# Kernel tuning notes

Hardware: AMD Instinct MI355X
Metric: run time of the kernel (lower is better)

The kernel has to match this reference:

```python
import jax, jax.numpy as jnp
import numpy as np

B, L0, L1, NS, D, H, NL, HM = 16, 512, 256, 32, 256, 8, 4, 4
T = L0 + L1 + NS + 1
HD = D // H
EPS = 1e-5
SCALE = HD ** -0.5


def setup_inputs() -> dict:
    key = jax.random.key(0)
    ks = jax.random.split(key, 20)
    s = 0.02
    return {
        'seq_tokens_0': jax.random.normal(ks[0], (B, L0, D), jnp.float32),
        'seq_tokens_1': jax.random.normal(ks[1], (B, L1, D), jnp.float32),
        'seq_lens_0': jax.random.randint(ks[2], (B,), 0, L0),
        'seq_lens_1': jax.random.randint(ks[3], (B,), 0, L1),
        'ns_tokens': jax.random.normal(ks[4], (B, NS, D), jnp.float32),
        'domain_emb': jax.random.normal(ks[5], (2, D), jnp.float32) * s,
        'cls_token': jax.random.normal(ks[6], (1, 1, D), jnp.float32) * s,
        'ln1_w': jnp.ones((NL, D), jnp.float32),
        'ln1_b': jnp.zeros((NL, D), jnp.float32),
        'qkv_w': jax.random.normal(ks[7], (NL, D, 3 * D), jnp.float32) * s,
        'qkv_b': jnp.zeros((NL, 3 * D), jnp.float32),
        'out_w': jax.random.normal(ks[8], (NL, D, D), jnp.float32) * s,
        'out_b': jnp.zeros((NL, D), jnp.float32),
        'ln2_w': jnp.ones((NL, D), jnp.float32),
        'ln2_b': jnp.zeros((NL, D), jnp.float32),
        'ffn1_w': jax.random.normal(ks[9], (NL, D, HM * D), jnp.float32) * s,
        'ffn1_b': jnp.zeros((NL, HM * D), jnp.float32),
        'ffn2_w': jax.random.normal(ks[10], (NL, HM * D, D), jnp.float32) * s,
        'ffn2_b': jnp.zeros((NL, D), jnp.float32),
        'fln_w': jnp.ones((D,), jnp.float32),
        'fln_b': jnp.zeros((D,), jnp.float32),
    }


def _ln(x, w, b):
    m = jnp.mean(x, -1, keepdims=True)
    v = jnp.var(x, -1, keepdims=True)
    return (x - m) * jax.lax.rsqrt(v + EPS) * w + b


def _build_mask(seq_lens_0, seq_lens_1):
    # static block structure: intra-domain causal, S<->NS bidirectional, CLS sink row
    base = jnp.zeros((T, T), bool)
    base = base.at[:L0, :L0].set(jnp.tril(jnp.ones((L0, L0), bool)))
    base = base.at[L0:L0 + L1, L0:L0 + L1].set(jnp.tril(jnp.ones((L1, L1), bool)))
    ns_s, ns_e = L0 + L1, L0 + L1 + NS
    base = base.at[:ns_s, ns_s:ns_e].set(True)   # S -> NS
    base = base.at[ns_s:ns_e, :ns_e].set(True)   # NS -> S and NS -> NS
    base = base.at[T - 1, :ns_e].set(True)       # CLS reads all S/NS
    base = base.at[T - 1, T - 1].set(True)       # CLS reads itself
    # per-batch padding mask on keys of each seq segment
    kv = jnp.ones((B, T), bool)
    kv = kv.at[:, :L0].set(jnp.arange(L0)[None, :] < seq_lens_0[:, None])
    kv = kv.at[:, L0:L0 + L1].set(jnp.arange(L1)[None, :] < seq_lens_1[:, None])
    return base[None] & kv[:, None, :]  # [B, T, T]


def _attention(x, mask, qkv_w, qkv_b, out_w, out_b):
    qkv = (x @ qkv_w + qkv_b).reshape(B, T, 3, H, HD)
    q, k, v = qkv[:, :, 0], qkv[:, :, 1], qkv[:, :, 2]
    scores = jnp.einsum('bqhd,bkhd->bhqk', q, k) * SCALE
    m = mask[:, None]  # [B,1,T,T]
    s = jnp.where(m, scores, -jnp.inf)
    any_valid = jnp.any(m, -1, keepdims=True)
    mx = jnp.where(any_valid, jnp.max(s, -1, keepdims=True), 0.0)
    e = jnp.exp(s - mx)  # masked entries exp(-inf)=0
    denom = jnp.sum(e, -1, keepdims=True)
    probs = e / jnp.maximum(denom, 1e-30)  # fully-masked rows -> zeros
    out = jnp.einsum('bhqk,bkhd->bqhd', probs, v).reshape(B, T, D)
    return out @ out_w + out_b


def reference(seq_tokens_0, seq_tokens_1, seq_lens_0, seq_lens_1, ns_tokens,
              domain_emb, cls_token, ln1_w, ln1_b, qkv_w, qkv_b, out_w, out_b,
              ln2_w, ln2_b, ffn1_w, ffn1_b, ffn2_w, ffn2_b, fln_w, fln_b):
    t0 = seq_tokens_0 + domain_emb[0][None, None, :]
    t1 = seq_tokens_1 + domain_emb[1][None, None, :]
    cls = jnp.broadcast_to(cls_token, (B, 1, D))
    x = jnp.concatenate([t0, t1, ns_tokens, cls], axis=1)  # [B,T,D]
    mask = _build_mask(seq_lens_0, seq_lens_1)
    for l in range(NL):
        x = x + _attention(_ln(x, ln1_w[l], ln1_b[l]), mask,
                           qkv_w[l], qkv_b[l], out_w[l], out_b[l])
        h = _ln(x, ln2_w[l], ln2_b[l])
        h = jax.nn.gelu(h @ ffn1_w[l] + ffn1_b[l], approximate=False)
        x = x + h @ ffn2_w[l] + ffn2_b[l]
    x = _ln(x, fln_w, fln_b)
    return x[:, -1, :]  # CLS state [B,D]
```

## Files before the change

### kernel.cpp

```cpp
#include <hip/hip_runtime.h>
#include <hip/hip_bf16.h>
#include <math.h>

typedef __attribute__((ext_vector_type(8))) unsigned short ushort8;
typedef __attribute__((ext_vector_type(8))) short short8;
typedef __attribute__((ext_vector_type(4))) float f32x4;
typedef __attribute__((ext_vector_type(4))) unsigned short ushort4v;
typedef __attribute__((ext_vector_type(4))) int i32x4;
typedef unsigned int u32;

namespace {
constexpr int B = 16, L0 = 512, L1 = 256, NS = 32, D = 256, H = 8, NL = 4, HM = 4;
constexpr int T = L0 + L1 + NS + 1;
constexpr int HD = D / H;
constexpr int NTOK = B * T;
constexpr int NS_S = L0 + L1;
constexpr int NS_E = NS_S + NS;
constexpr int TPAD = 832;
constexpr float EPS = 1e-5f;
constexpr float SCL2  = 0.17677669529663687f * 1.4426950408889634f;
}

__device__ __forceinline__ ushort f2bf(float f) {
    union { float f; unsigned u; } v; v.f = f;
    return (ushort)((v.u + 0x7fffu + ((v.u >> 16) & 1u)) >> 16);
}

__device__ __forceinline__ u32 cvtpk(float a, float b) {
    u32 r;
    asm("v_cvt_pk_bf16_f32 %0, %1, %2" : "=v"(r) : "v"(a), "v"(b));
    return r;
}

__device__ __forceinline__ void gload_lds16(const void* g, void* l) {
    __builtin_amdgcn_global_load_lds(
        (const __attribute__((address_space(1))) u32*)g,
        (__attribute__((address_space(3))) u32*)l, 16, 0, 0);
}

__device__ __forceinline__ bool any_valid_rows(
    int m0, int rows, const int* __restrict__ len0, const int* __restrict__ len1)
{
    int m1 = m0 + rows; if (m1 > NTOK) m1 = NTOK;
    const int b0 = m0 / T, b1 = (m1 - 1) / T;
    for (int b = b0; b <= b1; ++b) {
        int t0 = m0 - b * T; if (t0 < 0) t0 = 0;
        int t1 = m1 - b * T; if (t1 > T) t1 = T;
        if (t0 < len0[b]) return true;
        if (t1 > L0 && t0 < L0 + len1[b]) return true;
        if (t1 > NS_S) return true;
    }
    return false;
}

__global__ __launch_bounds__(256) void k_wprep_all(
    const float* __restrict__ qkvw, const float* __restrict__ outw,
    const float* __restrict__ f1w, const float* __restrict__ f2w,
    ushort* __restrict__ qkvt, ushort* __restrict__ outt,
    ushort* __restrict__ f1t, ushort* __restrict__ f2t)
{
    int id = blockIdx.x;
    const float* src; ushort* dst; int K, N;
    if (id < 768)        { src = qkvw; dst = qkvt; K = 256;  N = 768;  }
    else if (id < 1024)  { id -= 768;  src = outw; dst = outt; K = 256; N = 256; }
    else if (id < 2048)  { id -= 1024; src = f1w;  dst = f1t;  K = 256; N = 1024; }
    else                 { id -= 2048; src = f2w;  dst = f2t;  K = 1024; N = 256; }
    const int ktiles = K >> 5, per = ktiles * (N >> 5);
    const int layer = id / per, rem = id % per;
    const int kb = (rem % ktiles) * 32, nb = (rem / ktiles) * 32;
    src += (size_t)layer * K * N; dst += (size_t)layer * K * N;

    __shared__ float t[32][33];
    const int c = threadIdx.x & 31, r8 = threadIdx.x >> 5;
#pragma unroll
    for (int rr = 0; rr < 32; rr += 8)
        t[r8 + rr][c] = src[(size_t)(kb + r8 + rr) * N + nb + c];
    __syncthreads();
#pragma unroll
    for (int rr = 0; rr < 32; rr += 8)
        dst[(size_t)(nb + r8 + rr) * K + kb + c] = f2bf(t[c][r8 + rr]);
}

__global__ __launch_bounds__(256) void k_build_ln(
    const float* __restrict__ s0, const float* __restrict__ s1,
    const float* __restrict__ ns, const float* __restrict__ dom,
    const float* __restrict__ cls, const float* __restrict__ lnw,
    const float* __restrict__ lnb, float* __restrict__ x, ushort* __restrict__ xn)
{
    const int wid = threadIdx.x >> 6, lane = threadIdx.x & 63;
    const int row = blockIdx.x * 4 + wid;
    if (row >= NTOK) return;
    const int b = row / T, t = row % T;
    const int d0 = lane * 4;
    float4 v;
    if (t < L0) {
        v = *(const float4*)(s0 + ((size_t)b * L0 + t) * D + d0);
        float4 dm = *(const float4*)(dom + d0);
        v.x += dm.x; v.y += dm.y; v.z += dm.z; v.w += dm.w;
    } else if (t < NS_S) {
        v = *(const float4*)(s1 + ((size_t)b * L1 + (t - L0)) * D + d0);
        float4 dm = *(const float4*)(dom + D + d0);
        v.x += dm.x; v.y += dm.y; v.z += dm.z; v.w += dm.w;
    } else if (t < NS_E) {
        v = *(const float4*)(ns + ((size_t)b * NS + (t - NS_S)) * D + d0);
    } else {
        v = *(const float4*)(cls + d0);
    }
    *(float4*)(x + (size_t)row * D + d0) = v;
    float s  = v.x + v.y + v.z + v.w;
    float ss = v.x * v.x + v.y * v.y + v.z * v.z + v.w * v.w;
#pragma unroll
    for (int o = 32; o; o >>= 1) { s += __shfl_xor(s, o); ss += __shfl_xor(ss, o); }
    const float mean = s * (1.f / D);
    const float var  = ss * (1.f / D) - mean * mean;
    const float r = rsqrtf(var + EPS);
    float4 wv = *(const float4*)(lnw + d0);
    float4 bv = *(const float4*)(lnb + d0);
    ushort4v o4;
    o4[0] = f2bf((v.x - mean) * r * wv.x + bv.x);
    o4[1] = f2bf((v.y - mean) * r * wv.y + bv.y);
    o4[2] = f2bf((v.z - mean) * r * wv.z + bv.z);
    o4[3] = f2bf((v.w - mean) * r * wv.w + bv.w);
    *(ushort4v*)(xn + (size_t)row * D + d0) = o4;
}

template<bool GELU, bool RES, bool OBF, bool CLSW>
__global__ __launch_bounds__(256) void k_gemm_mfma(
    const ushort* __restrict__ A, const ushort* __restrict__ Wt,
    const float* __restrict__ bias, void* __restrict__ Cout,
    const float* __restrict__ res, const int* __restrict__ len0,
    const int* __restrict__ len1, int M, int N, int K, int nOff)
{
    __shared__ ushort As[2][128 * 64];
    __shared__ ushort Bs[2][128 * 64];
    const int tid = threadIdx.x;
    const int lane = tid & 63, w = tid >> 6;
    const int lo = lane & 15, g = lane >> 4;
    const int wr = w >> 1, wc = w & 1;
    const int m0 = CLSW ? (((blockIdx.x * T + (T - 1)) >> 7) << 7) : blockIdx.x * 128;
    const int n0 = (blockIdx.y + nOff) * 128;

    if (!CLSW && !any_valid_rows(m0, 128, len0, len1)) return;

    f32x4 zero = {0.f, 0.f, 0.f, 0.f};
    f32x4 acc[4][4];
#pragma unroll
    for (int mi = 0; mi < 4; ++mi)
#pragma unroll
        for (int ni = 0; ni < 4; ++ni) acc[mi][ni] = zero;

    const ushort* srcA[4];
    const ushort* srcB[4];
    int ldsOff[4];
#pragma unroll
    for (int i = 0; i < 4; ++i) {
        const int idx16 = (w * 4 + i) * 64 + lane;
        const int row = idx16 >> 3;
        const int scb = ((idx16 & 7) * 16) ^ ((row & 7) << 4);
        int arow = m0 + row; if (arow >= M) arow = M - 1;
        srcA[i] = A  + (size_t)arow * K + (scb >> 1);
        srcB[i] = Wt + (size_t)(n0 + row) * K + (scb >> 1);
        ldsOff[i] = (w * 4 + i) * 512;
    }

    const int NT = K >> 6;
#pragma unroll
    for (int i = 0; i < 4; ++i) {
        gload_lds16(srcA[i], &As[0][ldsOff[i]]);
        gload_lds16(srcB[i], &Bs[0][ldsOff[i]]);
    }
    asm volatile("s_waitcnt vmcnt(0)");
    __syncthreads();

    for (int t = 0; t < NT; ++t) {
        const int buf = t & 1;
        if (t + 1 < NT) {
            const int nb = buf ^ 1, ko = (t + 1) * 64;
#pragma unroll
            for (int i = 0; i < 4; ++i) {
                gload_lds16(srcA[i] + ko, &As[nb][ldsOff[i]]);
                gload_lds16(srcB[i] + ko, &Bs[nb][ldsOff[i]]);
            }
        }
#pragma unroll
        for (int kk = 0; kk < 2; ++kk) {
            const int kb = (kk * 64 + g * 16) ^ ((lo & 7) << 4);
            short8 af[4], bfr[4];
#pragma unroll
            for (int mi = 0; mi < 4; ++mi)
                af[mi] = *(const short8*)&As[buf][(wr * 64 + mi * 16 + lo) * 64 + (kb >> 1)];
#pragma unroll
            for (int ni = 0; ni < 4; ++ni)
                bfr[ni] = *(const short8*)&Bs[buf][(wc * 64 + ni * 16 + lo) * 64 + (kb >> 1)];
#pragma unroll
            for (int mi = 0; mi < 4; ++mi)
#pragma unroll
                for (int ni = 0; ni < 4; ++ni)
                    acc[mi][ni] = __builtin_amdgcn_mfma_f32_16x16x32_bf16(
                        af[mi], bfr[ni], acc[mi][ni], 0, 0, 0);
        }
        asm volatile("s_waitcnt vmcnt(0)");
        __syncthreads();
    }

    float bv[4];
#pragma unroll
    for (int ni = 0; ni < 4; ++ni) bv[ni] = bias[n0 + wc * 64 + ni * 16 + lo];
#pragma unroll
    for (int mi = 0; mi < 4; ++mi) {
#pragma unroll
        for (int i = 0; i < 4; ++i) {
            const int row = m0 + wr * 64 + mi * 16 + g * 4 + i;
            if (row >= M) continue;
#pragma unroll
            for (int ni = 0; ni < 4; ++ni) {
                const int col = n0 + wc * 64 + ni * 16 + lo;
                float v = acc[mi][ni][i] + bv[ni];
                if (GELU) v = 0.5f * v * (1.0f + erff(v * 0.70710678118654752f));
                if (RES)  v += res[(size_t)row * N + col];
                if (OBF) ((ushort*)Cout)[(size_t)row * N + col] = f2bf(v);
                else     ((float*)Cout)[(size_t)row * N + col] = v;
            }
        }
    }
}

template<int MODE, bool CLSW>
__global__ __launch_bounds__(256) void k_gemm_fused(
    const ushort* __restrict__ A, const ushort* __restrict__ Wt,
    const float* __restrict__ bias, const float* __restrict__ res,
    const float* __restrict__ lnw, const float* __restrict__ lnb,
    float* __restrict__ xout, ushort* __restrict__ xnout,
    float* __restrict__ dout, const int* __restrict__ len0,
    const int* __restrict__ len1, int M, int K)
{
    __shared__ ushort As[2][64 * 64];
    __shared__ ushort Bs[2][256 * 64];
    __shared__ float redS[64][4];
    __shared__ float redQ[64][4];
    const int tid = threadIdx.x;
    const int lane = tid & 63, w = tid >> 6;
    const int lo = lane & 15, g = lane >> 4;
    const int m0 = CLSW ? (((blockIdx.x * T + (T - 1)) >> 6) << 6) : blockIdx.x * 64;

    if (!CLSW && !any_valid_rows(m0, 64, len0, len1)) return;

    f32x4 zero = {0.f, 0.f, 0.f, 0.f};
    f32x4 acc[4][4];
#pragma unroll
    for (int mi = 0; mi < 4; ++mi)
#pragma unroll
        for (int ni = 0; ni < 4; ++ni) acc[mi][ni] = zero;

    const ushort* srcA[2]; int ldsOffA[2];
    const ushort* srcB[8]; int ldsOffB[8];
#pragma unroll
    for (int j = 0; j < 2; ++j) {
        const int idx16 = j * 256 + tid;
        const int row = idx16 >> 3;
        const int scb = ((idx16 & 7) * 16) ^ ((row & 7) << 4);
        int arow = m0 + row; if (arow >= M) arow = M - 1;
        srcA[j] = A + (size_t)arow * K + (scb >> 1);
        ldsOffA[j] = idx16 * 8;
    }
#pragma unroll
    for (int j = 0; j < 8; ++j) {
        const int idx16 = j * 256 + tid;
        const int row = idx16 >> 3;
        const int scb = ((idx16 & 7) * 16) ^ ((row & 7) << 4);
        srcB[j] = Wt + (size_t)row * K + (scb >> 1);
        ldsOffB[j] = idx16 * 8;
    }

    const int NT = K >> 6;
#pragma unroll
    for (int j = 0; j < 2; ++j) gload_lds16(srcA[j], &As[0][ldsOffA[j]]);
#pragma unroll
    for (int j = 0; j < 8; ++j) gload_lds16(srcB[j], &Bs[0][ldsOffB[j]]);
    asm volatile("s_waitcnt vmcnt(0)");
    __syncthreads();

    for (int t = 0; t < NT; ++t) {
        const int buf = t & 1;
        if (t + 1 < NT) {
            const int nb = buf ^ 1, ko = (t + 1) * 64;
#pragma unroll
            for (int j = 0; j < 2; ++j) gload_lds16(srcA[j] + ko, &As[nb][ldsOffA[j]]);
#pragma unroll
            for (int j = 0; j < 8; ++j) gload_lds16(srcB[j] + ko, &Bs[nb][ldsOffB[j]]);
        }
#pragma unroll
        for (int kk = 0; kk < 2; ++kk) {
            const int kb = (kk * 64 + g * 16) ^ ((lo & 7) << 4);
            short8 af[4], bfr[4];
#pragma unroll
            for (int mi = 0; mi < 4; ++mi)
                af[mi] = *(const short8*)&As[buf][(mi * 16 + lo) * 64 + (kb >> 1)];
#pragma unroll
            for (int ni = 0; ni < 4; ++ni)
                bfr[ni] = *(const short8*)&Bs[buf][(w * 64 + ni * 16 + lo) * 64 + (kb >> 1)];
#pragma unroll
            for (int mi = 0; mi < 4; ++mi)
#pragma unroll
                for (int ni = 0; ni < 4; ++ni)
                    acc[mi][ni] = __builtin_amdgcn_mfma_f32_16x16x32_bf16(
                        af[mi], bfr[ni], acc[mi][ni], 0, 0, 0);
        }
        asm volatile("s_waitcnt vmcnt(0)");
        __syncthreads();
    }

    float bv[4], lw[4], lb[4];
#pragma unroll
    for (int ni = 0; ni < 4; ++ni) {
        const int c = w * 64 + ni * 16 + lo;
        bv[ni] = bias[c]; lw[ni] = lnw[c]; lb[ni] = lnb[c];
    }
#pragma unroll
    for (int mi = 0; mi < 4; ++mi) {
#pragma unroll
        for (int i = 0; i < 4; ++i) {
            const int r64 = mi * 16 + g * 4 + i;
            const int row = m0 + r64;
            float s = 0.f, q = 0.f;
            if (row < M) {
#pragma unroll
                for (int ni = 0; ni < 4; ++ni) {
                    const int col = w * 64 + ni * 16 + lo;
                    float v = acc[mi][ni][i] + bv[ni] + res[(size_t)row * 256 + col];
                    acc[mi][ni][i] = v;
                    s += v; q += v * v;
                }
                s += __shfl_xor(s, 1); q += __shfl_xor(q, 1);
                s += __shfl_xor(s, 2); q += __shfl_xor(q, 2);
                s += __shfl_xor(s, 4); q += __shfl_xor(q, 4);
                s += __shfl_xor(s, 8); q += __shfl_xor(q, 8);
                if (lo == 0) { redS[r64][w] = s; redQ[r64][w] = q; }
            }
        }
    }
    __syncthreads();
#pragma unroll
    for (int mi = 0; mi < 4; ++mi) {
#pragma unroll
        for (int i = 0; i < 4; ++i) {
            const int r64 = mi * 16 + g * 4 + i;
            const int row = m0 + r64;
            if (row >= M) continue;
            const float S = redS[r64][0] + redS[r64][1] + redS[r64][2] + redS[r64][3];
            const float Q = redQ[r64][0] + redQ[r64][1] + redQ[r64][2] + redQ[r64][3];
            const float mean = S * (1.f / 256.f);
            const float var  = Q * (1.f / 256.f) - mean * mean;
            const float rstd = rsqrtf(var + EPS);
            if (MODE == 0) {
#pragma unroll
                for (int ni = 0; ni < 4; ++ni) {
                    const int col = w * 64 + ni * 16 + lo;
                    const float v = acc[mi][ni][i];
                    xout[(size_t)row * 256 + col] = v;
                    xnout[(size_t)row * 256 + col] = f2bf((v - mean) * rstd * lw[ni] + lb[ni]);
                }
            } else {
                const int bq = row / T;
                const int tq = row - bq * T;
                if (tq == T - 1) {
#pragma unroll
                    for (int ni = 0; ni < 4; ++ni) {
                        const int col = w * 64 + ni * 16 + lo;
                        dout[(size_t)bq * 256 + col] =
                            (acc[mi][ni][i] - mean) * rstd * lw[ni] + lb[ni];
                    }
                }
            }
        }
    }
}

__global__ __launch_bounds__(256) void k_repack(
    const ushort* __restrict__ qkv, ushort* __restrict__ Kb, ushort* __restrict__ Vt,
    const int* __restrict__ len0, const int* __restrict__ len1)
{
    const int bh = blockIdx.x, tt = blockIdx.y;
    const int b = bh >> 3, h = bh & 7;
    const int t0 = tt * 64;
    if (tt < 8)       { if (t0 >= len0[b]) return; }
    else if (tt < 12) { if (t0 >= L0 + len1[b]) return; }
    const int tid = threadIdx.x;
    const int r = tid >> 2, c = tid & 3;
    const int t = t0 + r;
    __shared__ ushort vtile[64][40];
    ushort8 k8 = {0,0,0,0,0,0,0,0}, v8 = {0,0,0,0,0,0,0,0};
    if (t < T) {
        const ushort* kp = qkv + ((size_t)(b * T + t) * 3 + 1) * D + h * HD + c * 8;
        k8 = *(const ushort8*)kp;
        v8 = *(const ushort8*)(kp + D);
    }
    *(ushort8*)(Kb + ((size_t)bh * TPAD + t0 + r) * HD + c * 8) = k8;
    *(ushort8*)&vtile[r][c * 8] = v8;
    __syncthreads();
    const int d = tid >> 3, cc = tid & 7;
    ushort8 o;
#pragma unroll
    for (int j = 0; j < 8; ++j) o[j] = vtile[cc * 8 + j][d];
    *(ushort8*)(Vt + ((size_t)bh * HD + d) * TPAD + t0 + cc * 8) = o;
}

__global__ __launch_bounds__(256) void k_flash(
    const ushort* __restrict__ qkv, const ushort* __restrict__ Kb,
    const ushort* __restrict__ Vt, const int* __restrict__ len0,
    const int* __restrict__ len1, ushort* __restrict__ out)
{
    const int bh = blockIdx.x;
    const int qt = 12 - blockIdx.y;
    const int b = bh >> 3, h = bh & 7;
    const int l0b = len0[b], lim01 = L0 + len1[b];

    const int q0t = qt * 64;
    if (qt < 8)       { if (q0t >= l0b) return; }
    else if (qt < 12) { if (q0t >= lim01) return; }

    const int tid = threadIdx.x, lane = tid & 63, w = tid >> 6;
    const int lo = lane & 15, g = lane >> 4;
    const int b4 = g & 1, b5 = g >> 1;
    const int q = q0t + w * 16 + lo;

    int klo = 0, klim;
    if (q < L0)        klim = q;
    else if (q < NS_S) { klo = L0; klim = q; }
    else if (q < NS_E) klim = NS_E - 1;
    else               klim = q;

    int qrow = q; if (qrow > T - 1) qrow = T - 1;
    short8 qf = *(const short8*)(qkv + ((size_t)(b * T + qrow) * 3) * D + h * HD + g * 8);

    const ushort* Kbase = Kb + (size_t)bh * TPAD * HD;
    const ushort* Vbase = Vt + (size_t)bh * HD * TPAD;

    f32x4 acc0 = {0.f, 0.f, 0.f, 0.f}, acc1 = {0.f, 0.f, 0.f, 0.f};
    float mrow = -1e30f, srow = 0.f;

    const int lt0 = (l0b + 63) >> 6;
    const int lt1 = (lim01 - L0 + 63) >> 6;
    int nc0, nc1;
    if (qt < 8)       { nc0 = min(qt + 1, lt0); nc1 = 0; }
    else if (qt < 12) { nc0 = 0; nc1 = min(qt - 7, lt1); }
    else              { nc0 = lt0; nc1 = lt1; }
    const int ntiles = nc0 + nc1 + 1;
    auto ktile = [&](int it) { return (it < nc0) ? it : (it < nc0 + nc1) ? (8 + it - nc0) : 12; };

    auto maskrow = [&](int k0, int n, const f32x4& sn, float pv[4], float& tmax) {
#pragma unroll
        for (int i = 0; i < 4; ++i) {
            const int k = k0 + n * 16 + g * 4 + i;
            const bool inNS = (k >= NS_S) & (k < NS_E);
            const bool kval = (k < l0b) | ((k >= L0) & (k < lim01)) | (k >= NS_S);
            const bool m = ((k >= klo) & (k <= klim) & kval) | inNS;
            const float sv = m ? sn[i] * SCL2 : -1e30f;
            pv[i] = sv;
            tmax = fmaxf(tmax, sv);
        }
    };
    auto xpose = [&](const u32 C0[4], const u32 C1[4], short8& pb0, short8& pb1) {
        u32 pb0u[4], pb1u[4];
#pragma unroll
        for (int n = 0; n < 4; ++n) {
            const u32 F0 = (u32)__shfl_xor((int)C0[n], 16);
            const u32 F1 = (u32)__shfl_xor((int)C1[n], 16);
            const u32 G00 = b4 ? F0 : C0[n];
            const u32 G01 = b4 ? C0[n] : F0;
            const u32 G10 = b4 ? F1 : C1[n];
            const u32 G11 = b4 ? C1[n] : F1;
            const u32 H00 = (u32)__shfl_xor((int)G00, 32);
            const u32 H01 = (u32)__shfl_xor((int)G01, 32);
            const u32 H10 = (u32)__shfl_xor((int)G10, 32);
            const u32 H11 = (u32)__shfl_xor((int)G11, 32);
            const bool keep = (b5 == b4);
            const u32 S00 = keep ? G00 : H00;
            const u32 S01 = keep ? G01 : H01;
            const u32 S10 = keep ? G10 : H10;
            const u32 S11 = keep ? G11 : H11;
            const bool take = (b5 == (n & 1));
            if ((n >> 1) == 0) {
                pb0u[0] = take ? S00 : pb0u[0];
                pb0u[1] = take ? S10 : pb0u[1];
                pb0u[2] = take ? S01 : pb0u[2];
                pb0u[3] = take ? S11 : pb0u[3];
            } else {
                pb1u[0] = take ? S00 : pb1u[0];
                pb1u[1] = take ? S10 : pb1u[1];
                pb1u[2] = take ? S01 : pb1u[2];
                pb1u[3] = take ? S11 : pb1u[3];
            }
        }
        i32x4 t0 = { (int)pb0u[0], (int)pb0u[1], (int)pb0u[2], (int)pb0u[3] };
        i32x4 t1 = { (int)pb1u[0], (int)pb1u[1], (int)pb1u[2], (int)pb1u[3] };
        pb0 = __builtin_bit_cast(short8, t0);
        pb1 = __builtin_bit_cast(short8, t1);
    };

    for (int it = 0; it < ntiles; ) {
        const bool has2 = (it + 1 < ntiles);
        const int kA = ktile(it) * 64;
        const int kB = has2 ? ktile(it + 1) * 64 : kA;

        short8 kfA[4], kfB[4];
#pragma unroll
        for (int n = 0; n < 4; ++n)
            kfA[n] = *(const short8*)(Kbase + (size_t)(kA + n * 16 + lo) * HD + g * 8);
        if (has2) {
#pragma unroll
            for (int n = 0; n < 4; ++n)
                kfB[n] = *(const short8*)(Kbase + (size_t)(kB + n * 16 + lo) * HD + g * 8);
        }

        const ushort* VA = Vbase + kA;
        short8 a00 = *(const short8*)(VA + (size_t)lo * TPAD + g * 8);
        short8 a01 = *(const short8*)(VA + (size_t)lo * TPAD + 32 + g * 8);
        short8 a10 = *(const short8*)(VA + (size_t)(16 + lo) * TPAD + g * 8);
        short8 a11 = *(const short8*)(VA + (size_t)(16 + lo) * TPAD + 32 + g * 8);
        short8 e00, e01, e10, e11;
        if (has2) {
            const ushort* VB = Vbase + kB;
            e00 = *(const short8*)(VB + (size_t)lo * TPAD + g * 8);
            e01 = *(const short8*)(VB + (size_t)lo * TPAD + 32 + g * 8);
            e10 = *(const short8*)(VB + (size_t)(16 + lo) * TPAD + g * 8);
            e11 = *(const short8*)(VB + (size_t)(16 + lo) * TPAD + 32 + g * 8);
        }

        float pvA[4][4], pvB[4][4];
        float tmax = -1e30f;
#pragma unroll
        for (int n = 0; n < 4; ++n) {
            f32x4 z = {0.f, 0.f, 0.f, 0.f};
            f32x4 sn = __builtin_amdgcn_mfma_f32_16x16x32_bf16(kfA[n], qf, z, 0, 0, 0);
            maskrow(kA, n, sn, pvA[n], tmax);
        }
        if (has2) {
#pragma unroll
            for (int n = 0; n < 4; ++n) {
                f32x4 z = {0.f, 0.f, 0.f, 0.f};
                f32x4 sn = __builtin_amdgcn_mfma_f32_16x16x32_bf16(kfB[n], qf, z, 0, 0, 0);
                maskrow(kB, n, sn, pvB[n], tmax);
            }
        }

        tmax = fmaxf(tmax, __shfl_xor(tmax, 16));
        tmax = fmaxf(tmax, __shfl_xor(tmax, 32));
        const float mnew = fmaxf(mrow, tmax);
        if (mnew > mrow) {
            const float scl = exp2f(mrow - mnew);
            srow *= scl;
#pragma unroll
            for (int i = 0; i < 4; ++i) { acc0[i] *= scl; acc1[i] *= scl; }
            mrow = mnew;
        }

        u32 CA0[4], CA1[4], CB0[4], CB1[4];
        float psum = 0.f;
#pragma unroll
        for (int n = 0; n < 4; ++n) {
            float e0 = exp2f(pvA[n][0] - mrow);
            float e1 = exp2f(pvA[n][1] - mrow);
            float e2 = exp2f(pvA[n][2] - mrow);
            float e3 = exp2f(pvA[n][3] - mrow);
            psum += (e0 + e1) + (e2 + e3);
            CA0[n] = cvtpk(e0, e1);
            CA1[n] = cvtpk(e2, e3);
        }
        if (has2) {
#pragma unroll
            for (int n = 0; n < 4; ++n) {
                float e0 = exp2f(pvB[n][0] - mrow);
                float e1 = exp2f(pvB[n][1] - mrow);
                float e2 = exp2f(pvB[n][2] - mrow);
                float e3 = exp2f(pvB[n][3] - mrow);
                psum += (e0 + e1) + (e2 + e3);
                CB0[n] = cvtpk(e0, e1);
                CB1[n] = cvtpk(e2, e3);
            }
        }
        psum += __shfl_xor(psum, 16);
        psum += __shfl_xor(psum, 32);
        srow += psum;

        short8 pb0, pb1;
        xpose(CA0, CA1, pb0, pb1);
        acc0 = __builtin_amdgcn_mfma_f32_16x16x32_bf16(a00, pb0, acc0, 0, 0, 0);
        acc0 = __builtin_amdgcn_mfma_f32_16x16x32_bf16(a01, pb1, acc0, 0, 0, 0);
        acc1 = __builtin_amdgcn_mfma_f32_16x16x32_bf16(a10, pb0, acc1, 0, 0, 0);
        acc1 = __builtin_amdgcn_mfma_f32_16x16x32_bf16(a11, pb1, acc1, 0, 0, 0);
        if (has2) {
            xpose(CB0, CB1, pb0, pb1);
            acc0 = __builtin_amdgcn_mfma_f32_16x16x32_bf16(e00, pb0, acc0, 0, 0, 0);
            acc0 = __builtin_amdgcn_mfma_f32_16x16x32_bf16(e01, pb1, acc0, 0, 0, 0);
            acc1 = __builtin_amdgcn_mfma_f32_16x16x32_bf16(e10, pb0, acc1, 0, 0, 0);
            acc1 = __builtin_amdgcn_mfma_f32_16x16x32_bf16(e11, pb1, acc1, 0, 0, 0);
        }

        it += has2 ? 2 : 1;
    }

    if (q < T) {
        const float inv = 1.f / fmaxf(srow, 1e-30f);
        ushort* orow = out + (size_t)(b * T + q) * D + h * HD;
        *(u32*)(orow + g * 4)          = cvtpk(acc0[0] * inv, acc0[1] * inv);
        *(u32*)(orow + g * 4 + 2)      = cvtpk(acc0[2] * inv, acc0[3] * inv);
        *(u32*)(orow + 16 + g * 4)     = cvtpk(acc1[0] * inv, acc1[1] * inv);
        *(u32*)(orow + 16 + g * 4 + 2) = cvtpk(acc1[2] * inv, acc1[3] * inv);
    }
}

extern "C" void kernel_launch(void* const* d_in, const int* in_sizes, int n_in,
                              void* d_out, int out_size, void* d_ws, size_t ws_size,
                              hipStream_t stream)
{
    const float* seq0 = (const float*)d_in[0];
    const float* seq1 = (const float*)d_in[1];
    const int*   len0 = (const int*)d_in[2];
    const int*   len1 = (const int*)d_in[3];
    const float* nst  = (const float*)d_in[4];
    const float* dom  = (const float*)d_in[5];
    const float* cls  = (const float*)d_in[6];
    const float* ln1w = (const float*)d_in[7];
    const float* ln1b = (const float*)d_in[8];
    const float* qkvw = (const float*)d_in[9];
    const float* qkvb = (const float*)d_in[10];
    const float* outw = (const float*)d_in[11];
    const float* outb = (const float*)d_in[12];
    const float* ln2w = (const float*)d_in[13];
    const float* ln2b = (const float*)d_in[14];
    const float* f1w  = (const float*)d_in[15];
    const float* f1b  = (const float*)d_in[16];
    const float* f2w  = (const float*)d_in[17];
    const float* f2b  = (const float*)d_in[18];
    const float* flnw = (const float*)d_in[19];
    const float* flnb = (const float*)d_in[20];

    float*  x   = (float*)d_ws;
    ushort* xn  = (ushort*)(x + (size_t)NTOK * D);
    ushort* big = xn + (size_t)NTOK * D;
    ushort* Kb  = big + (size_t)NTOK * HM * D;
    ushort* Vt  = Kb + (size_t)B * H * TPAD * HD;
    ushort* qkvw_t = Vt + (size_t)B * H * TPAD * HD;
    ushort* outw_t = qkvw_t + (size_t)NL * 768 * 256;
    ushort* f1w_t  = outw_t + (size_t)NL * 256 * 256;
    ushort* f2w_t  = f1w_t  + (size_t)NL * 1024 * 256;

    k_wprep_all<<<3072, 256, 0, stream>>>(qkvw, outw, f1w, f2w,
                                          qkvw_t, outw_t, f1w_t, f2w_t);

    k_build_ln<<<(NTOK + 3) / 4, 256, 0, stream>>>(seq0, seq1, nst, dom, cls,
                                                   ln1w, ln1b, x, xn);

    const int gmm = (NTOK + 127) / 128;
    const int gf  = (NTOK + 63) / 64;

    for (int l = 0; l < NL; ++l) {
        const bool last = (l == NL - 1);
        if (!last) {
            k_gemm_mfma<false, false, true, false><<<dim3(gmm, 6), 256, 0, stream>>>(
                xn, qkvw_t + (size_t)l * 768 * 256, qkvb + (size_t)l * 3 * D, big, nullptr,
                len0, len1, NTOK, 3 * D, D, 0);
        } else {
            k_gemm_mfma<false, false, true, false><<<dim3(gmm, 4), 256, 0, stream>>>(
                xn, qkvw_t + (size_t)l * 768 * 256, qkvb + (size_t)l * 3 * D, big, nullptr,
                len0, len1, NTOK, 3 * D, D, 2);
            k_gemm_mfma<false, false, true, true><<<dim3(B, 2), 256, 0, stream>>>(
                xn, qkvw_t + (size_t)l * 768 * 256, qkvb + (size_t)l * 3 * D, big, nullptr,
                len0, len1, NTOK, 3 * D, D, 0);
        }
        k_repack<<<dim3(B * H, TPAD / 64), 256, 0, stream>>>(big, Kb, Vt, len0, len1);
        k_flash<<<dim3(B * H, last ? 1 : TPAD / 64), 256, 0, stream>>>(
            big, Kb, Vt, len0, len1, xn);
        if (!last)
            k_gemm_fused<0, false><<<gf, 256, 0, stream>>>(
                xn, outw_t + (size_t)l * 256 * 256, outb + (size_t)l * D, x,
                ln2w + l * D, ln2b + l * D, x, xn, nullptr, len0, len1, NTOK, D);
        else
            k_gemm_fused<0, true><<<B, 256, 0, stream>>>(
                xn, outw_t + (size_t)l * 256 * 256, outb + (size_t)l * D, x,
                ln2w + l * D, ln2b + l * D, x, xn, nullptr, len0, len1, NTOK, D);
        if (!last)
            k_gemm_mfma<true, false, true, false><<<dim3(gmm, 8), 256, 0, stream>>>(
                xn, f1w_t + (size_t)l * 1024 * 256, f1b + (size_t)l * HM * D, big,
                nullptr, len0, len1, NTOK, HM * D, D, 0);
        else
            k_gemm_mfma<true, false, true, true><<<dim3(B, 8), 256, 0, stream>>>(
                xn, f1w_t + (size_t)l * 1024 * 256, f1b + (size_t)l * HM * D, big,
                nullptr, len0, len1, NTOK, HM * D, D, 0);
        if (!last)
            k_gemm_fused<0, false><<<gf, 256, 0, stream>>>(
                big, f2w_t + (size_t)l * 256 * 1024, f2b + (size_t)l * D, x,
                ln1w + (l + 1) * D, ln1b + (l + 1) * D, x, xn, nullptr, len0, len1,
                NTOK, HM * D);
        else
            k_gemm_fused<1, true><<<B, 256, 0, stream>>>(
                big, f2w_t + (size_t)l * 256 * 1024, f2b + (size_t)l * D, x,
                flnw, flnb, nullptr, nullptr, (float*)d_out, len0, len1, NTOK, HM * D);
    }
}
```

Baseline: 479.6 us.

## Compact valid tokens into packed per-batch rows, skipping masked padding

```diff
diff --git a/kernel.cpp b/kernel.cpp
--- a/kernel.cpp
+++ b/kernel.cpp
@@ -13,10 +13,9 @@
 constexpr int B = 16, L0 = 512, L1 = 256, NS = 32, D = 256, H = 8, NL = 4, HM = 4;
 constexpr int T = L0 + L1 + NS + 1;
 constexpr int HD = D / H;
-constexpr int NTOK = B * T;
 constexpr int NS_S = L0 + L1;
-constexpr int NS_E = NS_S + NS;
 constexpr int TPAD = 832;
+constexpr int ROWP = 13312;
 constexpr float EPS = 1e-5f;
 constexpr float SCL2  = 0.17677669529663687f * 1.4426950408889634f;
 }
@@ -38,19 +37,39 @@
         (__attribute__((address_space(3))) u32*)l, 16, 0, 0);
 }
 
-__device__ __forceinline__ bool any_valid_rows(
-    int m0, int rows, const int* __restrict__ len0, const int* __restrict__ len1)
+__global__ __launch_bounds__(256) void k_idx(
+    const int* __restrict__ len0, const int* __restrict__ len1,
+    int* __restrict__ offs, int* __restrict__ rowinfo)
 {
-    int m1 = m0 + rows; if (m1 > NTOK) m1 = NTOK;
-    const int b0 = m0 / T, b1 = (m1 - 1) / T;
-    for (int b = b0; b <= b1; ++b) {
-        int t0 = m0 - b * T; if (t0 < 0) t0 = 0;
-        int t1 = m1 - b * T; if (t1 > T) t1 = T;
-        if (t0 < len0[b]) return true;
-        if (t1 > L0 && t0 < L0 + len1[b]) return true;
-        if (t1 > NS_S) return true;
-    }
-    return false;
+    __shared__ int so[17];
+    const int tid = threadIdx.x;
+    if (tid == 0) {
+        int acc = 0;
+        for (int b = 0; b < 16; ++b) {
+            so[b] = acc;
+            const int nv = len0[b] + len1[b] + 33;
+            acc += ((nv + 63) >> 6) << 6;
+        }
+        so[16] = acc;
+    }
+    __syncthreads();
+    if (tid < 17) offs[tid] = so[tid];
+    for (int r = tid; r < ROWP; r += 256) {
+        int info = -1;
+        if (r < so[16]) {
+            int b = 15;
+            for (int j = 0; j < 15; ++j) if (r < so[j + 1]) { b = j; break; }
+            const int loc = r - so[b];
+            const int n0 = len0[b], n1 = len1[b];
+            if (loc < n0 + n1 + 33) {
+                const int t = (loc < n0) ? loc
+                            : (loc < n0 + n1) ? (L0 + loc - n0)
+                            : (NS_S + loc - n0 - n1);
+                info = (b << 16) | t;
+            }
+        }
+        rowinfo[r] = info;
+    }
 }
 
 __global__ __launch_bounds__(256) void k_wprep_all(
@@ -85,13 +104,22 @@
     const float* __restrict__ s0, const float* __restrict__ s1,
     const float* __restrict__ ns, const float* __restrict__ dom,
     const float* __restrict__ cls, const float* __restrict__ lnw,
-    const float* __restrict__ lnb, float* __restrict__ x, ushort* __restrict__ xn)
+    const float* __restrict__ lnb, const int* __restrict__ rowinfo,
+    float* __restrict__ x, ushort* __restrict__ xn)
 {
     const int wid = threadIdx.x >> 6, lane = threadIdx.x & 63;
     const int row = blockIdx.x * 4 + wid;
-    if (row >= NTOK) return;
-    const int b = row / T, t = row % T;
+    if (row >= ROWP) return;
     const int d0 = lane * 4;
+    const int info = rowinfo[row];
+    if (info < 0) {
+        float4 z = {0.f, 0.f, 0.f, 0.f};
+        *(float4*)(x + (size_t)row * D + d0) = z;
+        ushort4v z4 = {0, 0, 0, 0};
+        *(ushort4v*)(xn + (size_t)row * D + d0) = z4;
+        return;
+    }
+    const int b = info >> 16, t = info & 0xFFFF;
     float4 v;
     if (t < L0) {
         v = *(const float4*)(s0 + ((size_t)b * L0 + t) * D + d0);
@@ -101,7 +129,7 @@
         v = *(const float4*)(s1 + ((size_t)b * L1 + (t - L0)) * D + d0);
         float4 dm = *(const float4*)(dom + D + d0);
         v.x += dm.x; v.y += dm.y; v.z += dm.z; v.w += dm.w;
-    } else if (t < NS_E) {
+    } else if (t < NS_S + NS) {
         v = *(const float4*)(ns + ((size_t)b * NS + (t - NS_S)) * D + d0);
     } else {
         v = *(const float4*)(cls + d0);
@@ -124,12 +152,12 @@
     *(ushort4v*)(xn + (size_t)row * D + d0) = o4;
 }
 
-template<bool GELU, bool RES, bool OBF, bool CLSW>
+template<bool GELU, bool OBF, bool CLSW>
 __global__ __launch_bounds__(256) void k_gemm_mfma(
     const ushort* __restrict__ A, const ushort* __restrict__ Wt,
     const float* __restrict__ bias, void* __restrict__ Cout,
-    const float* __restrict__ res, const int* __restrict__ len0,
-    const int* __restrict__ len1, int M, int N, int K, int nOff)
+    const int* __restrict__ offs, const int* __restrict__ len0,
+    const int* __restrict__ len1, int N, int K, int nOff)
 {
     __shared__ ushort As[2][128 * 64];
     __shared__ ushort Bs[2][128 * 64];
@@ -137,10 +165,16 @@
     const int lane = tid & 63, w = tid >> 6;
     const int lo = lane & 15, g = lane >> 4;
     const int wr = w >> 1, wc = w & 1;
-    const int m0 = CLSW ? (((blockIdx.x * T + (T - 1)) >> 7) << 7) : blockIdx.x * 128;
+    int m0;
+    if (CLSW) {
+        const int bb = blockIdx.x;
+        const int clsrow = offs[bb] + len0[bb] + len1[bb] + 32;
+        m0 = (clsrow >> 7) << 7;
+    } else {
+        m0 = blockIdx.x * 128;
+        if (m0 >= offs[16]) return;
+    }
     const int n0 = (blockIdx.y + nOff) * 128;
-
-    if (!CLSW && !any_valid_rows(m0, 128, len0, len1)) return;
 
     f32x4 zero = {0.f, 0.f, 0.f, 0.f};
     f32x4 acc[4][4];
@@ -157,8 +191,7 @@
         const int idx16 = (w * 4 + i) * 64 + lane;
         const int row = idx16 >> 3;
         const int scb = ((idx16 & 7) * 16) ^ ((row & 7) << 4);
-        int arow = m0 + row; if (arow >= M) arow = M - 1;
-        srcA[i] = A  + (size_t)arow * K + (scb >> 1);
+        srcA[i] = A  + (size_t)(m0 + row) * K + (scb >> 1);
         srcB[i] = Wt + (size_t)(n0 + row) * K + (scb >> 1);
         ldsOff[i] = (w * 4 + i) * 512;
     }
@@ -211,13 +244,11 @@
 #pragma unroll
         for (int i = 0; i < 4; ++i) {
             const int row = m0 + wr * 64 + mi * 16 + g * 4 + i;
-            if (row >= M) continue;
 #pragma unroll
             for (int ni = 0; ni < 4; ++ni) {
                 const int col = n0 + wc * 64 + ni * 16 + lo;
                 float v = acc[mi][ni][i] + bv[ni];
                 if (GELU) v = 0.5f * v * (1.0f + erff(v * 0.70710678118654752f));
-                if (RES)  v += res[(size_t)row * N + col];
                 if (OBF) ((ushort*)Cout)[(size_t)row * N + col] = f2bf(v);
                 else     ((float*)Cout)[(size_t)row * N + col] = v;
             }
@@ -231,8 +262,9 @@
     const float* __restrict__ bias, const float* __restrict__ res,
     const float* __restrict__ lnw, const float* __restrict__ lnb,
     float* __restrict__ xout, ushort* __restrict__ xnout,
-    float* __restrict__ dout, const int* __restrict__ len0,
-    const int* __restrict__ len1, int M, int K)
+    float* __restrict__ dout, const int* __restrict__ offs,
+    const int* __restrict__ rowinfo, const int* __restrict__ len0,
+    const int* __restrict__ len1, int K)
 {
     __shared__ ushort As[2][64 * 64];
     __shared__ ushort Bs[2][256 * 64];
@@ -241,9 +273,15 @@
     const int tid = threadIdx.x;
     const int lane = tid & 63, w = tid >> 6;
     const int lo = lane & 15, g = lane >> 4;
-    const int m0 = CLSW ? (((blockIdx.x * T + (T - 1)) >> 6) << 6) : blockIdx.x * 64;
-
-    if (!CLSW && !any_valid_rows(m0, 64, len0, len1)) return;
+    int m0;
+    if (CLSW) {
+        const int bb = blockIdx.x;
+        const int clsrow = offs[bb] + len0[bb] + len1[bb] + 32;
+        m0 = (clsrow >> 6) << 6;
+    } else {
+        m0 = blockIdx.x * 64;
+        if (m0 >= offs[16]) return;
+    }
 
     f32x4 zero = {0.f, 0.f, 0.f, 0.f};
     f32x4 acc[4][4];
@@ -259,8 +297,7 @@
         const int idx16 = j * 256 + tid;
         const int row = idx16 >> 3;
         const int scb = ((idx16 & 7) * 16) ^ ((row & 7) << 4);
-        int arow = m0 + row; if (arow >= M) arow = M - 1;
-        srcA[j] = A + (size_t)arow * K + (scb >> 1);
+        srcA[j] = A + (size_t)(m0 + row) * K + (scb >> 1);
         ldsOffA[j] = idx16 * 8;
     }
 #pragma unroll
@@ -323,20 +360,18 @@
             const int r64 = mi * 16 + g * 4 + i;
             const int row = m0 + r64;
             float s = 0.f, q = 0.f;
-            if (row < M) {
-#pragma unroll
-                for (int ni = 0; ni < 4; ++ni) {
-                    const int col = w * 64 + ni * 16 + lo;
-                    float v = acc[mi][ni][i] + bv[ni] + res[(size_t)row * 256 + col];
-                    acc[mi][ni][i] = v;
-                    s += v; q += v * v;
-                }
-                s += __shfl_xor(s, 1); q += __shfl_xor(q, 1);
-                s += __shfl_xor(s, 2); q += __shfl_xor(q, 2);
-                s += __shfl_xor(s, 4); q += __shfl_xor(q, 4);
-                s += __shfl_xor(s, 8); q += __shfl_xor(q, 8);
-                if (lo == 0) { redS[r64][w] = s; redQ[r64][w] = q; }
+#pragma unroll
+            for (int ni = 0; ni < 4; ++ni) {
+                const int col = w * 64 + ni * 16 + lo;
+                float v = acc[mi][ni][i] + bv[ni] + res[(size_t)row * 256 + col];
+                acc[mi][ni][i] = v;
+                s += v; q += v * v;
             }
+            s += __shfl_xor(s, 1); q += __shfl_xor(q, 1);
+            s += __shfl_xor(s, 2); q += __shfl_xor(q, 2);
+            s += __shfl_xor(s, 4); q += __shfl_xor(q, 4);
+            s += __shfl_xor(s, 8); q += __shfl_xor(q, 8);
+            if (lo == 0) { redS[r64][w] = s; redQ[r64][w] = q; }
         }
     }
     __syncthreads();
@@ -346,7 +381,6 @@
         for (int i = 0; i < 4; ++i) {
             const int r64 = mi * 16 + g * 4 + i;
             const int row = m0 + r64;
-            if (row >= M) continue;
             const float S = redS[r64][0] + redS[r64][1] + redS[r64][2] + redS[r64][3];
             const float Q = redQ[r64][0] + redQ[r64][1] + redQ[r64][2] + redQ[r64][3];
             const float mean = S * (1.f / 256.f);
@@ -361,9 +395,9 @@
                     xnout[(size_t)row * 256 + col] = f2bf((v - mean) * rstd * lw[ni] + lb[ni]);
                 }
             } else {
-                const int bq = row / T;
-                const int tq = row - bq * T;
-                if (tq == T - 1) {
+                const int info = rowinfo[row];
+                if (info >= 0 && (info & 0xFFFF) == T - 1) {
+                    const int bq = info >> 16;
 #pragma unroll
                     for (int ni = 0; ni < 4; ++ni) {
                         const int col = w * 64 + ni * 16 + lo;
@@ -378,23 +412,21 @@
 
 __global__ __launch_bounds__(256) void k_repack(
     const ushort* __restrict__ qkv, ushort* __restrict__ Kb, ushort* __restrict__ Vt,
-    const int* __restrict__ len0, const int* __restrict__ len1)
+    const int* __restrict__ offs, const int* __restrict__ len0,
+    const int* __restrict__ len1)
 {
     const int bh = blockIdx.x, tt = blockIdx.y;
     const int b = bh >> 3, h = bh & 7;
+    const int nv = len0[b] + len1[b] + 33;
     const int t0 = tt * 64;
-    if (tt < 8)       { if (t0 >= len0[b]) return; }
-    else if (tt < 12) { if (t0 >= L0 + len1[b]) return; }
+    if (t0 >= nv) return;
+    const int base = offs[b];
     const int tid = threadIdx.x;
     const int r = tid >> 2, c = tid & 3;
-    const int t = t0 + r;
     __shared__ ushort vtile[64][40];
-    ushort8 k8 = {0,0,0,0,0,0,0,0}, v8 = {0,0,0,0,0,0,0,0};
-    if (t < T) {
-        const ushort* kp = qkv + ((size_t)(b * T + t) * 3 + 1) * D + h * HD + c * 8;
-        k8 = *(const ushort8*)kp;
-        v8 = *(const ushort8*)(kp + D);
-    }
+    const ushort* kp = qkv + (size_t)(base + t0 + r) * 768 + 256 + h * HD + c * 8;
+    ushort8 k8 = *(const ushort8*)kp;
+    ushort8 v8 = *(const ushort8*)(kp + 256);
     *(ushort8*)(Kb + ((size_t)bh * TPAD + t0 + r) * HD + c * 8) = k8;
     *(ushort8*)&vtile[r][c * 8] = v8;
     __syncthreads();
@@ -405,33 +437,30 @@
     *(ushort8*)(Vt + ((size_t)bh * HD + d) * TPAD + t0 + cc * 8) = o;
 }
 
+template<bool CLSONLY>
 __global__ __launch_bounds__(256) void k_flash(
     const ushort* __restrict__ qkv, const ushort* __restrict__ Kb,
-    const ushort* __restrict__ Vt, const int* __restrict__ len0,
-    const int* __restrict__ len1, ushort* __restrict__ out)
+    const ushort* __restrict__ Vt, const int* __restrict__ offs,
+    const int* __restrict__ len0, const int* __restrict__ len1,
+    ushort* __restrict__ out)
 {
     const int bh = blockIdx.x;
-    const int qt = 12 - blockIdx.y;
     const int b = bh >> 3, h = bh & 7;
-    const int l0b = len0[b], lim01 = L0 + len1[b];
-
-    const int q0t = qt * 64;
-    if (qt < 8)       { if (q0t >= l0b) return; }
-    else if (qt < 12) { if (q0t >= lim01) return; }
-
+    const int clen0 = len0[b], cns = clen0 + len1[b];
+    const int nv = cns + 33;
+    const int tl = (nv - 1) >> 6, tn0 = cns >> 6;
+    int qt;
+    if (CLSONLY) qt = tl;
+    else { qt = 12 - (int)blockIdx.y; if (qt > tl) return; }
+
+    const int base = offs[b];
     const int tid = threadIdx.x, lane = tid & 63, w = tid >> 6;
     const int lo = lane & 15, g = lane >> 4;
     const int b4 = g & 1, b5 = g >> 1;
+    const int q0t = qt * 64;
     const int q = q0t + w * 16 + lo;
 
-    int klo = 0, klim;
-    if (q < L0)        klim = q;
-    else if (q < NS_S) { klo = L0; klim = q; }
-    else if (q < NS_E) klim = NS_E - 1;
-    else               klim = q;
-
-    int qrow = q; if (qrow > T - 1) qrow = T - 1;
-    short8 qf = *(const short8*)(qkv + ((size_t)(b * T + qrow) * 3) * D + h * HD + g * 8);
+    short8 qf = *(const short8*)(qkv + (size_t)(base + q) * 768 + h * HD + g * 8);
 
     const ushort* Kbase = Kb + (size_t)bh * TPAD * HD;
     const ushort* Vbase = Vt + (size_t)bh * HD * TPAD;
@@ -439,22 +468,23 @@
     f32x4 acc0 = {0.f, 0.f, 0.f, 0.f}, acc1 = {0.f, 0.f, 0.f, 0.f};
     float mrow = -1e30f, srow = 0.f;
 
-    const int lt0 = (l0b + 63) >> 6;
-    const int lt1 = (lim01 - L0 + 63) >> 6;
-    int nc0, nc1;
-    if (qt < 8)       { nc0 = min(qt + 1, lt0); nc1 = 0; }
-    else if (qt < 12) { nc0 = 0; nc1 = min(qt - 7, lt1); }
-    else              { nc0 = lt0; nc1 = lt1; }
-    const int ntiles = nc0 + nc1 + 1;
-    auto ktile = [&](int it) { return (it < nc0) ? it : (it < nc0 + nc1) ? (8 + it - nc0) : 12; };
+    const int kts = (q0t >= clen0 && (q0t + 63) < cns) ? (clen0 >> 6) : 0;
+    const int nc = qt - kts + 1;
+    const int estart = (qt + 1 > tn0) ? (qt + 1) : tn0;
+    const int extra = (tl >= estart) ? (tl - estart + 1) : 0;
+    const int ntiles = nc + extra;
+    auto ktile = [&](int it) { return (it < nc) ? (kts + it) : (estart + (it - nc)); };
 
     auto maskrow = [&](int k0, int n, const f32x4& sn, float pv[4], float& tmax) {
 #pragma unroll
         for (int i = 0; i < 4; ++i) {
             const int k = k0 + n * 16 + g * 4 + i;
-            const bool inNS = (k >= NS_S) & (k < NS_E);
-            const bool kval = (k < l0b) | ((k >= L0) & (k < lim01)) | (k >= NS_S);
-            const bool m = ((k >= klo) & (k <= klim) & kval) | inNS;
+            const bool win = (k >= cns) & (k < cns + 32);
+            bool m;
+            if (q < clen0)         m = (k <= q) | win;
+            else if (q < cns)      m = ((k >= clen0) & (k <= q)) | win;
+            else if (q < cns + 32) m = (k < cns + 32);
+            else                   m = (k < cns + 32) | (k == q);
             const float sv = m ? sn[i] * SCL2 : -1e30f;
             pv[i] = sv;
             tmax = fmaxf(tmax, sv);
@@ -559,10 +589,10 @@
         float psum = 0.f;
 #pragma unroll
         for (int n = 0; n < 4; ++n) {
-            float e0 = exp2f(pvA[n][0] - mrow);
-            float e1 = exp2f(pvA[n][1] - mrow);
-            float e2 = exp2f(pvA[n][2] - mrow);
-            float e3 = exp2f(pvA[n][3] - mrow);
+            float e0 = (pvA[n][0] > -1e29f) ? exp2f(pvA[n][0] - mrow) : 0.f;
+            float e1 = (pvA[n][1] > -1e29f) ? exp2f(pvA[n][1] - mrow) : 0.f;
+            float e2 = (pvA[n][2] > -1e29f) ? exp2f(pvA[n][2] - mrow) : 0.f;
+            float e3 = (pvA[n][3] > -1e29f) ? exp2f(pvA[n][3] - mrow) : 0.f;
             psum += (e0 + e1) + (e2 + e3);
             CA0[n] = cvtpk(e0, e1);
             CA1[n] = cvtpk(e2, e3);
@@ -570,10 +600,10 @@
         if (has2) {
 #pragma unroll
             for (int n = 0; n < 4; ++n) {
-                float e0 = exp2f(pvB[n][0] - mrow);
-                float e1 = exp2f(pvB[n][1] - mrow);
-                float e2 = exp2f(pvB[n][2] - mrow);
-                float e3 = exp2f(pvB[n][3] - mrow);
+                float e0 = (pvB[n][0] > -1e29f) ? exp2f(pvB[n][0] - mrow) : 0.f;
+                float e1 = (pvB[n][1] > -1e29f) ? exp2f(pvB[n][1] - mrow) : 0.f;
+                float e2 = (pvB[n][2] > -1e29f) ? exp2f(pvB[n][2] - mrow) : 0.f;
+                float e3 = (pvB[n][3] > -1e29f) ? exp2f(pvB[n][3] - mrow) : 0.f;
                 psum += (e0 + e1) + (e2 + e3);
                 CB0[n] = cvtpk(e0, e1);
                 CB1[n] = cvtpk(e2, e3);
@@ -600,9 +630,9 @@
         it += has2 ? 2 : 1;
     }
 
-    if (q < T) {
+    if (q < nv) {
         const float inv = 1.f / fmaxf(srow, 1e-30f);
-        ushort* orow = out + (size_t)(b * T + q) * D + h * HD;
+        ushort* orow = out + (size_t)(base + q) * D + h * HD;
         *(u32*)(orow + g * 4)          = cvtpk(acc0[0] * inv, acc0[1] * inv);
         *(u32*)(orow + g * 4 + 2)      = cvtpk(acc0[2] * inv, acc0[3] * inv);
         *(u32*)(orow + 16 + g * 4)     = cvtpk(acc1[0] * inv, acc1[1] * inv);
@@ -637,65 +667,74 @@
     const float* flnb = (const float*)d_in[20];
 
     float*  x   = (float*)d_ws;
-    ushort* xn  = (ushort*)(x + (size_t)NTOK * D);
-    ushort* big = xn + (size_t)NTOK * D;
-    ushort* Kb  = big + (size_t)NTOK * HM * D;
+    ushort* xn  = (ushort*)(x + (size_t)ROWP * D);
+    ushort* big = xn + (size_t)ROWP * D;
+    ushort* Kb  = big + (size_t)ROWP * HM * D;
     ushort* Vt  = Kb + (size_t)B * H * TPAD * HD;
     ushort* qkvw_t = Vt + (size_t)B * H * TPAD * HD;
     ushort* outw_t = qkvw_t + (size_t)NL * 768 * 256;
     ushort* f1w_t  = outw_t + (size_t)NL * 256 * 256;
     ushort* f2w_t  = f1w_t  + (size_t)NL * 1024 * 256;
+    int* offs      = (int*)(f2w_t + (size_t)NL * 256 * 1024);
+    int* rowinfo   = offs + 32;
 
     k_wprep_all<<<3072, 256, 0, stream>>>(qkvw, outw, f1w, f2w,
                                           qkvw_t, outw_t, f1w_t, f2w_t);
-
-    k_build_ln<<<(NTOK + 3) / 4, 256, 0, stream>>>(seq0, seq1, nst, dom, cls,
-                                                   ln1w, ln1b, x, xn);
-
-    const int gmm = (NTOK + 127) / 128;
-    const int gf  = (NTOK + 63) / 64;
+    k_idx<<<1, 256, 0, stream>>>(len0, len1, offs, rowinfo);
+    k_build_ln<<<ROWP / 4, 256, 0, stream>>>(seq0, seq1, nst, dom, cls,
+                                             ln1w, ln1b, rowinfo, x, xn);
+
+    const int gmm = ROWP / 128;
+    const int gf  = ROWP / 64;
 
     for (int l = 0; l < NL; ++l) {
         const bool last = (l == NL - 1);
         if (!last) {
-            k_gemm_mfma<false, false, true, false><<<dim3(gmm, 6), 256, 0, stream>>>(
-                xn, qkvw_t + (size_t)l * 768 * 256, qkvb + (size_t)l * 3 * D, big, nullptr,
-                len0, len1, NTOK, 3 * D, D, 0);
+            k_gemm_mfma<false, true, false><<<dim3(gmm, 6), 256, 0, stream>>>(
+                xn, qkvw_t + (size_t)l * 768 * 256, qkvb + (size_t)l * 3 * D, big,
+                offs, len0, len1, 3 * D, D, 0);
         } else {
-            k_gemm_mfma<false, false, true, false><<<dim3(gmm, 4), 256, 0, stream>>>(
-                xn, qkvw_t + (size_t)l * 768 * 256, qkvb + (size_t)l * 3 * D, big, nullptr,
-                len0, len1, NTOK, 3 * D, D, 2);
-            k_gemm_mfma<false, false, true, true><<<dim3(B, 2), 256, 0, stream>>>(
-                xn, qkvw_t + (size_t)l * 768 * 256, qkvb + (size_t)l * 3 * D, big, nullptr,
-                len0, len1, NTOK, 3 * D, D, 0);
-        }
-        k_repack<<<dim3(B * H, TPAD / 64), 256, 0, stream>>>(big, Kb, Vt, len0, len1);
-        k_flash<<<dim3(B * H, last ? 1 : TPAD / 64), 256, 0, stream>>>(
-            big, Kb, Vt, len0, len1, xn);
+            k_gemm_mfma<false, true, false><<<dim3(gmm, 4), 256, 0, stream>>>(
+                xn, qkvw_t + (size_t)l * 768 * 256, qkvb + (size_t)l * 3 * D, big,
+                offs, len0, len1, 3 * D, D, 2);
+            k_gemm_mfma<false, true, true><<<dim3(B, 2), 256, 0, stream>>>(
+                xn, qkvw_t + (size_t)l * 768 * 256, qkvb + (size_t)l * 3 * D, big,
+                offs, len0, len1, 3 * D, D, 0);
+        }
+        k_repack<<<dim3(B * H, 13), 256, 0, stream>>>(big, Kb, Vt, offs, len0, len1);
+        if (!last)
+            k_flash<false><<<dim3(B * H, 13), 256, 0, stream>>>(
+                big, Kb, Vt, offs, len0, len1, xn);
+        else
+            k_flash<true><<<dim3(B * H, 1), 256, 0, stream>>>(
+                big, Kb, Vt, offs, len0, len1, xn);
         if (!last)
             k_gemm_fused<0, false><<<gf, 256, 0, stream>>>(
                 xn, outw_t + (size_t)l * 256 * 256, outb + (size_t)l * D, x,
-                ln2w + l * D, ln2b + l * D, x, xn, nullptr, len0, len1, NTOK, D);
+                ln2w + l * D, ln2b + l * D, x, xn, nullptr, offs, rowinfo,
+                len0, len1, D);
         else
             k_gemm_fused<0, true><<<B, 256, 0, stream>>>(
                 xn, outw_t + (size_t)l * 256 * 256, outb + (size_t)l * D, x,
-                ln2w + l * D, ln2b + l * D, x, xn, nullptr, len0, len1, NTOK, D);
+                ln2w + l * D, ln2b + l * D, x, xn, nullptr, offs, rowinfo,
+                len0, len1, D);
         if (!last)
-            k_gemm_mfma<true, false, true, false><<<dim3(gmm, 8), 256, 0, stream>>>(
+            k_gemm_mfma<true, true, false><<<dim3(gmm, 8), 256, 0, stream>>>(
                 xn, f1w_t + (size_t)l * 1024 * 256, f1b + (size_t)l * HM * D, big,
-                nullptr, len0, len1, NTOK, HM * D, D, 0);
+                offs, len0, len1, HM * D, D, 0);
         else
-            k_gemm_mfma<true, false, true, true><<<dim3(B, 8), 256, 0, stream>>>(
+            k_gemm_mfma<true, true, true><<<dim3(B, 8), 256, 0, stream>>>(
                 xn, f1w_t + (size_t)l * 1024 * 256, f1b + (size_t)l * HM * D, big,
-                nullptr, len0, len1, NTOK, HM * D, D, 0);
+                offs, len0, len1, HM * D, D, 0);
         if (!last)
             k_gemm_fused<0, false><<<gf, 256, 0, stream>>>(
                 big, f2w_t + (size_t)l * 256 * 1024, f2b + (size_t)l * D, x,
-                ln1w + (l + 1) * D, ln1b + (l + 1) * D, x, xn, nullptr, len0, len1,
-                NTOK, HM * D);
+                ln1w + (l + 1) * D, ln1b + (l + 1) * D, x, xn, nullptr, offs,
+                rowinfo, len0, len1, HM * D);
         else
             k_gemm_fused<1, true><<<B, 256, 0, stream>>>(
                 big, f2w_t + (size_t)l * 256 * 1024, f2b + (size_t)l * D, x,
-                flnw, flnb, nullptr, nullptr, (float*)d_out, len0, len1, NTOK, HM * D);
-    }
-}
+                flnw, flnb, nullptr, nullptr, (float*)d_out, offs, rowinfo,
+                len0, len1, HM * D);
+    }
+}
```

Measured after the change: 465.1 us. -3.0%, faster.
